# Kernel optimization log

Measured on AMD Instinct MI355X. Metric: run time of the kernel, lower is better.

## Reference

```python
import jax, jax.numpy as jnp
import numpy as np

B, C, H, W = 4, 64, 256, 512


def setup_inputs() -> dict:
    key = jax.random.key(0)
    k1, k2 = jax.random.split(key)
    input1 = jax.random.normal(k1, (B, C, H, W), dtype=jnp.float32)
    # horizontal displacement field (pixels)
    input2 = jax.random.normal(k2, (B, 1, H, W), dtype=jnp.float32)
    return {"input1": input1, "input2": input2}


def reference(input1, input2):
    # 1D (along-width) bilinear resampling: out[b,c,h,w] = input1 sampled at x = w + disp[b,h,w]
    b, c, h, w = input1.shape
    disp = input2[:, 0]                                   # [B,H,W]
    x = jnp.arange(w, dtype=input1.dtype) + disp          # sample coords [B,H,W]
    valid = ((x >= 0) & (x <= w - 1)).astype(input1.dtype)
    x0 = jnp.floor(x)
    frac = x - x0                                         # bilinear weight
    i0 = jnp.clip(x0, 0, w - 1).astype(jnp.int32)
    i1 = jnp.clip(x0 + 1, 0, w - 1).astype(jnp.int32)
    idx0 = jnp.broadcast_to(i0[:, None], (b, c, h, w))
    idx1 = jnp.broadcast_to(i1[:, None], (b, c, h, w))
    g0 = jnp.take_along_axis(input1, idx0, axis=3)
    g1 = jnp.take_along_axis(input1, idx1, axis=3)
    out = ((1.0 - frac)[:, None] * g0 + frac[:, None] * g1) * valid[:, None]
    return out
```

## Files before the change

### kernel.cpp

```cpp
#include <hip/hip_runtime.h>


#define B 4
#define C 64
#define H 256
#define W 512
#define WAVES 4
#define CPW 8

__global__ __launch_bounds__(256) void resample1d_kernel(
    const float* __restrict__ in1,
    const float* __restrict__ in2,
    float* __restrict__ out)
{
    __shared__ float rowbuf[WAVES][W];

    const int tid  = threadIdx.x;
    const int wid  = tid >> 6;
    const int lane = tid & 63;

    const int bh = blockIdx.x;
    const int b  = bh >> 8;
    const int h  = bh & (H - 1);
    const int cbase = blockIdx.y * (WAVES * CPW) + wid * CPW;

    const float* disp_row = in2 + (size_t)bh * W;
    int   i0[8], i1[8];
    float w0[8], w1[8];
    #pragma unroll
    for (int p = 0; p < 8; ++p) {
        int w = lane + 64 * p;
        float x = (float)w + disp_row[w];
        bool valid = (x >= 0.0f) && (x <= (float)(W - 1));
        float x0 = floorf(x);
        float frac = x - x0;
        float x0c = fminf(fmaxf(x0, 0.0f), (float)(W - 1));
        i0[p] = (int)x0c;
        i1[p] = min(i0[p] + 1, W - 1);
        w0[p] = valid ? (1.0f - frac) : 0.0f;
        w1[p] = valid ? frac : 0.0f;
    }

    float* rb = rowbuf[wid];

    const size_t chan_stride = (size_t)H * W;
    const float* src = in1 + ((size_t)b * C + cbase) * chan_stride + (size_t)h * W;
    float*       dst = out + ((size_t)b * C + cbase) * chan_stride + (size_t)h * W;

    float4 r0 = *(const float4*)(src + 4 * lane);
    float4 r1 = *(const float4*)(src + 256 + 4 * lane);

    #pragma unroll
    for (int cc = 0; cc < CPW; ++cc) {
        *(float4*)(rb + 4 * lane)       = r0;
        *(float4*)(rb + 256 + 4 * lane) = r1;
        if (cc + 1 < CPW) {
            const float* s2 = src + (size_t)(cc + 1) * chan_stride;
            r0 = *(const float4*)(s2 + 4 * lane);
            r1 = *(const float4*)(s2 + 256 + 4 * lane);
        }
        float* d = dst + (size_t)cc * chan_stride;
        #pragma unroll
        for (int p = 0; p < 8; ++p) {
            float g0 = rb[i0[p]];
            float g1 = rb[i1[p]];
            __builtin_nontemporal_store(w0[p] * g0 + w1[p] * g1, d + lane + 64 * p);
        }
    }
}

extern "C" void kernel_launch(void* const* d_in, const int* in_sizes, int n_in,
                              void* d_out, int out_size, void* d_ws, size_t ws_size,
                              hipStream_t stream) {
    const float* in1 = (const float*)d_in[0];
    const float* in2 = (const float*)d_in[1];
    float* out = (float*)d_out;

    dim3 grid(B * H, C / (WAVES * CPW)), block(WAVES * 64);
    resample1d_kernel<<<grid, block, 0, stream>>>(in1, in2, out);
}
```

Measured before the change: 47.86 us.

## Vectorize displacement loads and output stores, deepen channel prefetch to two

Each lane now handles four contiguous pixels instead of a strided set. This lets the displacement row be read with float4 loads and the output written with 128-bit nontemporal stores in place of scalar ones. The channel-row prefetch is now double-buffered two channels ahead, and the first two channels' loads are issued before the index/weight setup. The aim is to cut memory instruction count and hide global load latency, at the cost of more registers and possible LDS bank conflicts from contiguous per-lane gather addresses.

```diff
diff --git a/kernel.cpp b/kernel.cpp
--- a/kernel.cpp
+++ b/kernel.cpp
@@ -7,6 +7,8 @@
 #define W 512
 #define WAVES 4
 #define CPW 8
+
+typedef float f32x4 __attribute__((ext_vector_type(4)));
 
 __global__ __launch_bounds__(256) void resample1d_kernel(
     const float* __restrict__ in1,
@@ -21,50 +23,61 @@
 
     const int bh = blockIdx.x;
     const int b  = bh >> 8;
-    const int h  = bh & (H - 1);
     const int cbase = blockIdx.y * (WAVES * CPW) + wid * CPW;
 
+    const size_t chan_stride = (size_t)H * W;
+    const float* src = in1 + ((size_t)b * C + cbase) * chan_stride + (size_t)(bh & (H - 1)) * W;
+    float*       dst = out + ((size_t)b * C + cbase) * chan_stride + (size_t)(bh & (H - 1)) * W;
     const float* disp_row = in2 + (size_t)bh * W;
-    int   i0[8], i1[8];
-    float w0[8], w1[8];
+
+    f32x4 pre0[2], pre1[2];
+    pre0[0] = *(const f32x4*)(src + 4 * lane);
+    pre1[0] = *(const f32x4*)(src + 256 + 4 * lane);
+    pre0[1] = *(const f32x4*)(src + chan_stride + 4 * lane);
+    pre1[1] = *(const f32x4*)(src + chan_stride + 256 + 4 * lane);
+    f32x4 d4[2];
+    d4[0] = *(const f32x4*)(disp_row + 4 * lane);
+    d4[1] = *(const f32x4*)(disp_row + 256 + 4 * lane);
+
+    int   i0[2][4];
+    float w0[2][4], w1[2][4];
     #pragma unroll
-    for (int p = 0; p < 8; ++p) {
-        int w = lane + 64 * p;
-        float x = (float)w + disp_row[w];
-        bool valid = (x >= 0.0f) && (x <= (float)(W - 1));
-        float x0 = floorf(x);
-        float frac = x - x0;
-        float x0c = fminf(fmaxf(x0, 0.0f), (float)(W - 1));
-        i0[p] = (int)x0c;
-        i1[p] = min(i0[p] + 1, W - 1);
-        w0[p] = valid ? (1.0f - frac) : 0.0f;
-        w1[p] = valid ? frac : 0.0f;
+    for (int g = 0; g < 2; ++g) {
+        #pragma unroll
+        for (int j = 0; j < 4; ++j) {
+            int w = 4 * lane + 256 * g + j;
+            float x = (float)w + d4[g][j];
+            bool valid = (x >= 0.0f) && (x <= (float)(W - 1));
+            float x0 = floorf(x);
+            float frac = x - x0;
+            i0[g][j] = (int)fminf(fmaxf(x0, 0.0f), (float)(W - 1));
+            w0[g][j] = valid ? (1.0f - frac) : 0.0f;
+            w1[g][j] = valid ? frac : 0.0f;
+        }
     }
 
     float* rb = rowbuf[wid];
 
-    const size_t chan_stride = (size_t)H * W;
-    const float* src = in1 + ((size_t)b * C + cbase) * chan_stride + (size_t)h * W;
-    float*       dst = out + ((size_t)b * C + cbase) * chan_stride + (size_t)h * W;
-
-    float4 r0 = *(const float4*)(src + 4 * lane);
-    float4 r1 = *(const float4*)(src + 256 + 4 * lane);
-
     #pragma unroll
     for (int cc = 0; cc < CPW; ++cc) {
-        *(float4*)(rb + 4 * lane)       = r0;
-        *(float4*)(rb + 256 + 4 * lane) = r1;
-        if (cc + 1 < CPW) {
-            const float* s2 = src + (size_t)(cc + 1) * chan_stride;
-            r0 = *(const float4*)(s2 + 4 * lane);
-            r1 = *(const float4*)(s2 + 256 + 4 * lane);
+        *(f32x4*)(rb + 4 * lane)       = pre0[cc & 1];
+        *(f32x4*)(rb + 256 + 4 * lane) = pre1[cc & 1];
+        if (cc + 2 < CPW) {
+            const float* s2 = src + (size_t)(cc + 2) * chan_stride;
+            pre0[cc & 1] = *(const f32x4*)(s2 + 4 * lane);
+            pre1[cc & 1] = *(const f32x4*)(s2 + 256 + 4 * lane);
         }
         float* d = dst + (size_t)cc * chan_stride;
         #pragma unroll
-        for (int p = 0; p < 8; ++p) {
-            float g0 = rb[i0[p]];
-            float g1 = rb[i1[p]];
-            __builtin_nontemporal_store(w0[p] * g0 + w1[p] * g1, d + lane + 64 * p);
+        for (int g = 0; g < 2; ++g) {
+            f32x4 r;
+            #pragma unroll
+            for (int j = 0; j < 4; ++j) {
+                int a0 = i0[g][j];
+                int a1 = min(a0 + 1, W - 1);
+                r[j] = w0[g][j] * rb[a0] + w1[g][j] * rb[a1];
+            }
+            __builtin_nontemporal_store(r, (f32x4*)(d + 4 * lane + 256 * g));
         }
     }
 }
```

After: 45.85 us. -4.2%, faster.
